# Optimization experiments

Hardware: AMD Instinct MI355X
Metric: run time of the kernel (lower is better)

## Reference

```python
import jax, jax.numpy as jnp
import numpy as np

C_M = 256
C = 32
C_Z = 128
EPS = 1e-5


def setup_inputs() -> dict:
    key = jax.random.key(0)
    ks = jax.random.split(key, 8)
    b, s, i = 1, 128, 256
    msa = jax.random.normal(ks[0], (b, s, i, C_M), dtype=jnp.float32)
    scale_in = 1.0 / np.sqrt(C_M)
    scale_out = 1.0 / np.sqrt(C * C)
    return {
        "msa_representation": msa,
        "ln_w": jnp.ones((C_M,), jnp.float32),
        "ln_b": jnp.zeros((C_M,), jnp.float32),
        "w_left": jax.random.normal(ks[1], (C_M, C), jnp.float32) * scale_in,
        "b_left": jax.random.normal(ks[2], (C,), jnp.float32) * scale_in,
        "w_right": jax.random.normal(ks[3], (C_M, C), jnp.float32) * scale_in,
        "b_right": jax.random.normal(ks[4], (C,), jnp.float32) * scale_in,
        "w_out": jax.random.normal(ks[5], (C * C, C_Z), jnp.float32) * scale_out,
        "b_out": jax.random.normal(ks[6], (C_Z,), jnp.float32) * scale_out,
    }


def reference(msa_representation, ln_w, ln_b, w_left, b_left, w_right, b_right, w_out, b_out):
    x = msa_representation
    # LayerNorm over c_m
    mu = jnp.mean(x, axis=-1, keepdims=True)
    var = jnp.mean(jnp.square(x - mu), axis=-1, keepdims=True)
    x = (x - mu) * jax.lax.rsqrt(var + EPS) * ln_w + ln_b
    # dual projections: [b, s, i, c]
    A = x @ w_left + b_left
    B = x @ w_right + b_right
    s_dim = x.shape[1]
    # outer product mean over MSA depth s: [b, i, j, c, c]
    outer = jnp.einsum('bsic,bsjd->bijcd', A, B) / s_dim
    b_, i_, j_ = outer.shape[0], outer.shape[1], outer.shape[2]
    flat = outer.reshape(b_, i_, j_, C * C)
    return flat @ w_out + b_out
```

## Files before the change

### kernel.cpp

```cpp
#include <hip/hip_runtime.h>

typedef __attribute__((ext_vector_type(8))) short short8;
typedef __attribute__((ext_vector_type(4))) float f32x4;

#define CM 256
#define CC 32
#define CZ 128
#define SDIM 128
#define IDIM 256

__device__ __forceinline__ unsigned short f2bf(float f) {
  union { float f; unsigned u; } v; v.f = f;
  unsigned r = v.u + 0x7fffu + ((v.u >> 16) & 1u);
  return (unsigned short)(r >> 16);
}
__device__ __forceinline__ unsigned pack_bf2(float a, float b) {
  union { float f; unsigned u; } x, y; x.f = a; y.f = b;
  return ((x.u + 0x8000u) >> 16) | ((y.u + 0x8000u) & 0xffff0000u);
}

__global__ void k_prep(const float* __restrict__ wl, const float* __restrict__ wr,
                       const float* __restrict__ wo,
                       unsigned short* __restrict__ wlrT2, unsigned short* __restrict__ WF) {
  int t = blockIdx.x * 256 + threadIdx.x;
  if (t < 2048) {
    int frag = t >> 6, lane = t & 63;
    int nt = frag >> 3, ks = frag & 7;
    int ln = lane & 15, qd = lane >> 4;
    int c64 = nt * 16 + ln;
#pragma unroll
    for (int e = 0; e < 8; ++e) {
      int cm = ks * 32 + qd * 8 + e;
      float v = (c64 < CC) ? wl[cm * CC + c64] : wr[cm * CC + (c64 - CC)];
      wlrT2[(size_t)t * 8 + e] = f2bf(v);
    }
  } else {
    int t2 = t - 2048;
    if (t2 < 8 * 32 * 64) {
      int zt = t2 >> 11, ks = (t2 >> 6) & 31, lane = t2 & 63;
      int ln = lane & 15, qd = lane >> 4;
      int z = zt * 16 + ln;
#pragma unroll
      for (int e = 0; e < 8; ++e) {
        int c = qd * 8 + e, d = ks;
        WF[(size_t)t2 * 8 + e] = f2bf(wo[(c * 32 + d) * CZ + z] * (1.0f / 128.0f));
      }
    }
  }
}

__global__ __launch_bounds__(512) void k_lnproj(
    const float* __restrict__ x, const float* __restrict__ lnw, const float* __restrict__ lnb,
    const float* __restrict__ bl, const float* __restrict__ br,
    const unsigned short* __restrict__ wlrT2,
    unsigned short* __restrict__ A2, unsigned short* __restrict__ Bbuf) {
  __shared__ __align__(16) unsigned short xn[64][264];
  __shared__ __align__(16) unsigned short sT[64][72];
  int tid = threadIdx.x;
  int lane = tid & 63, ww = tid >> 6;
  int qd = lane >> 4, ln = lane & 15;
  int i = blockIdx.x, sh = blockIdx.y;

  float4 w4 = ((const float4*)lnw)[lane];
  float4 b4 = ((const float4*)lnb)[lane];

#pragma unroll
  for (int rr = 0; rr < 8; ++rr) {
    int sl = ww * 8 + rr;
    int s = sh * 64 + sl;
    float4 v = ((const float4*)(x + ((size_t)s * IDIM + i) * CM))[lane];
    float s1 = v.x + v.y + v.z + v.w;
    float s2 = v.x * v.x + v.y * v.y + v.z * v.z + v.w * v.w;
#pragma unroll
    for (int off = 32; off; off >>= 1) {
      s1 += __shfl_xor(s1, off);
      s2 += __shfl_xor(s2, off);
    }
    float mu = s1 * (1.0f / 256.0f);
    float var = s2 * (1.0f / 256.0f) - mu * mu;
    float rs = rsqrtf(var + 1e-5f);
    ushort4 h;
    h.x = f2bf((v.x - mu) * rs * w4.x + b4.x);
    h.y = f2bf((v.y - mu) * rs * w4.y + b4.y);
    h.z = f2bf((v.z - mu) * rs * w4.z + b4.z);
    h.w = f2bf((v.w - mu) * rs * w4.w + b4.w);
    *(ushort4*)&xn[sl][lane * 4] = h;
  }
  __syncthreads();

  int mt = ww >> 1, nh = ww & 1;
  f32x4 acc[2];
#pragma unroll
  for (int t = 0; t < 2; ++t) acc[t] = (f32x4){0.f, 0.f, 0.f, 0.f};
#pragma unroll
  for (int ks = 0; ks < 8; ++ks) {
    short8 af = *(const short8*)&xn[mt * 16 + ln][ks * 32 + qd * 8];
#pragma unroll
    for (int t = 0; t < 2; ++t) {
      int nt = nh * 2 + t;
      short8 bf = *(const short8*)(wlrT2 + ((size_t)((nt * 8 + ks) * 64 + lane)) * 8);
      acc[t] = __builtin_amdgcn_mfma_f32_16x16x32_bf16(af, bf, acc[t], 0, 0, 0);
    }
  }
#pragma unroll
  for (int t = 0; t < 2; ++t) {
    int nt = nh * 2 + t;
    int c64 = nt * 16 + ln;
    float bias = (c64 < CC) ? bl[c64] : br[c64 - CC];
    ushort4 h;
    h.x = f2bf(acc[t][0] + bias);
    h.y = f2bf(acc[t][1] + bias);
    h.z = f2bf(acc[t][2] + bias);
    h.w = f2bf(acc[t][3] + bias);
    *(ushort4*)&sT[c64][mt * 16 + qd * 4] = h;
  }
  __syncthreads();

  if (ww < 4) {
    int rtloc = ww >> 1, ksl = ww & 1;
    short8 v = *(const short8*)&sT[rtloc * 16 + ln][ksl * 32 + qd * 8];
    *(short8*)(A2 + ((size_t)(((2 * i + rtloc) * 4 + (sh * 2 + ksl)) * 64 + lane)) * 8) = v;
  } else {
    int t2 = tid - 256;
    int row = t2 >> 3, ch = t2 & 7;
    short8 v = *(const short8*)&sT[CC + row][ch * 8];
    *(short8*)(Bbuf + ((size_t)(i * CC + row)) * SDIM + sh * 64 + ch * 8) = v;
  }
}

__global__ __launch_bounds__(512, 2) void k_main(
    const unsigned short* __restrict__ A2, const unsigned short* __restrict__ Bbuf,
    const unsigned short* __restrict__ WF, const float* __restrict__ bout,
    float* __restrict__ out) {
  extern __shared__ __align__(16) char lds[];
  unsigned short* sPA = (unsigned short*)lds;
  unsigned short* sPB = (unsigned short*)(lds + 66048);
  unsigned short* sB  = (unsigned short*)(lds + 132096);
  float* redR = (float*)lds;
  int tid = threadIdx.x;
  int lane = tid & 63, ww = tid >> 6;
  int qd = lane >> 4, ln = lane & 15;
  int bx = blockIdx.x;
  int itile = (bx & 7) * 4 + ((bx >> 3) & 3);
  int jg = bx >> 5;
  int i0 = itile * 8;
  int ztp = ww & 3, kq = ww >> 2;

  short8 afp[2][4];
#pragma unroll
  for (int ti = 0; ti < 2; ++ti)
#pragma unroll
    for (int ks = 0; ks < 4; ++ks)
      afp[ti][ks] =
          *(const short8*)(A2 + ((size_t)((i0 * 2 + ww * 2 + ti) * 4 + ks) * 64 + lane) * 8);

  short8 bpre[2];
#pragma unroll
  for (int tt = 0; tt < 2; ++tt) {
    int idx = tid + tt * 512;
    int r = idx >> 4, ch = idx & 15;
    bpre[tt] = *(const short8*)(Bbuf + ((size_t)(jg * 256 + r)) * SDIM + ch * 8);
  }

#pragma unroll
  for (int q = 0; q < 4; ++q) {
#pragma unroll
    for (int tt = 0; tt < 2; ++tt) {
      int idx = tid + tt * 512;
      int r = idx >> 4, ch = idx & 15;
      *(short8*)&sB[r * 136 + ch * 8] = bpre[tt];
    }
    __syncthreads();
    if (q < 3) {
#pragma unroll
      for (int tt = 0; tt < 2; ++tt) {
        int idx = tid + tt * 512;
        int r = idx >> 4, ch = idx & 15;
        bpre[tt] = *(const short8*)(Bbuf + ((size_t)(jg * 256 + (q + 1) * 64 + r)) * SDIM + ch * 8);
      }
    }
    unsigned short* sP = (q & 2) ? sPB : sPA;
    f32x4 acc1[2][4];
#pragma unroll
    for (int a = 0; a < 2; ++a)
#pragma unroll
      for (int b = 0; b < 4; ++b) acc1[a][b] = (f32x4){0.f, 0.f, 0.f, 0.f};
#pragma unroll
    for (int ks = 0; ks < 4; ++ks)
#pragma unroll
      for (int tjj = 0; tjj < 4; ++tjj) {
        short8 bf = *(const short8*)&sB[(tjj * 16 + ln) * 136 + ks * 32 + qd * 8];
#pragma unroll
        for (int ti = 0; ti < 2; ++ti)
          acc1[ti][tjj] =
              __builtin_amdgcn_mfma_f32_16x16x32_bf16(afp[ti][ks], bf, acc1[ti][tjj], 0, 0, 0);
      }
    __syncthreads();
#pragma unroll
    for (int ti = 0; ti < 2; ++ti) {
      int cbase = 16 * ti + qd * 4;
      int cb = cbase >> 3;
#pragma unroll
      for (int tjj = 0; tjj < 4; ++tjj) {
        int d = 16 * (tjj & 1) + ln;
        int p = ww * 4 + 2 * (q & 1) + (tjj >> 1);
        uint2 u;
        u.x = pack_bf2(acc1[ti][tjj][0], acc1[ti][tjj][1]);
        u.y = pack_bf2(acc1[ti][tjj][2], acc1[ti][tjj][3]);
        *(uint2*)&sP[p * 1032 + d * 32 + ((((d >> 1) & 3) ^ cb) * 8) + (cbase & 7)] = u;
      }
    }
  }
  __syncthreads();

  f32x4 acc2[2][2][2];
#pragma unroll
  for (int a = 0; a < 2; ++a)
#pragma unroll
    for (int b = 0; b < 2; ++b)
#pragma unroll
      for (int c = 0; c < 2; ++c) acc2[a][b][c] = (f32x4){0.f, 0.f, 0.f, 0.f};
#pragma unroll
  for (int cc = 0; cc < 16; ++cc) {
    int ks = kq * 16 + cc;
    int swz = ((((ks >> 1) & 3) ^ qd) * 8);
    short8 afr[2][2];
#pragma unroll
    for (int mt = 0; mt < 2; ++mt) {
      afr[0][mt] = *(const short8*)&sPA[(mt * 16 + ln) * 1032 + ks * 32 + swz];
      afr[1][mt] = *(const short8*)&sPB[(mt * 16 + ln) * 1032 + ks * 32 + swz];
    }
#pragma unroll
    for (int h2 = 0; h2 < 2; ++h2) {
      int zt = ztp * 2 + h2;
      short8 bfr = *(const short8*)(WF + ((size_t)(zt * 32 + ks) * 64 + lane) * 8);
#pragma unroll
      for (int tb = 0; tb < 2; ++tb)
#pragma unroll
        for (int mt = 0; mt < 2; ++mt)
          acc2[tb][h2][mt] = __builtin_amdgcn_mfma_f32_16x16x32_bf16(bfr, afr[tb][mt],
                                                                    acc2[tb][h2][mt], 0, 0, 0);
    }
  }
  __syncthreads();

  if (kq == 1) {
#pragma unroll
    for (int tb = 0; tb < 2; ++tb)
#pragma unroll
      for (int h2 = 0; h2 < 2; ++h2)
#pragma unroll
        for (int mt = 0; mt < 2; ++mt)
          *(f32x4*)&redR[((((tb * 4 + ztp) * 2 + h2) * 2 + mt) << 8) + lane * 4] =
              acc2[tb][h2][mt];
  }
  __syncthreads();
  if (kq == 0) {
#pragma unroll
    for (int tb = 0; tb < 2; ++tb)
#pragma unroll
      for (int h2 = 0; h2 < 2; ++h2) {
        int z = (ztp * 2 + h2) * 16 + qd * 4;
        f32x4 bz = *(const f32x4*)(bout + z);
#pragma unroll
        for (int mt = 0; mt < 2; ++mt) {
          int p = mt * 16 + ln;
          f32x4 v = acc2[tb][h2][mt] +
                    *(const f32x4*)&redR[((((tb * 4 + ztp) * 2 + h2) * 2 + mt) << 8) + lane * 4] +
                    bz;
          int i = i0 + (p >> 2), j = jg * 8 + tb * 4 + (p & 3);
          *(f32x4*)&out[((size_t)i * IDIM + j) * CZ + z] = v;
        }
      }
  }
}

extern "C" void kernel_launch(void* const* d_in, const int* in_sizes, int n_in,
                              void* d_out, int out_size, void* d_ws, size_t ws_size,
                              hipStream_t stream) {
  const float* msa = (const float*)d_in[0];
  const float* lnw = (const float*)d_in[1];
  const float* lnb = (const float*)d_in[2];
  const float* wl  = (const float*)d_in[3];
  const float* bl  = (const float*)d_in[4];
  const float* wr  = (const float*)d_in[5];
  const float* br  = (const float*)d_in[6];
  const float* wo  = (const float*)d_in[7];
  const float* bo  = (const float*)d_in[8];
  float* out = (float*)d_out;

  char* ws = (char*)d_ws;
  unsigned short* A2    = (unsigned short*)ws;
  unsigned short* Bbuf  = (unsigned short*)(ws + (2u << 20));
  unsigned short* wlrT2 = (unsigned short*)(ws + (4u << 20));
  unsigned short* WF    = (unsigned short*)(ws + (4u << 20) + 32768);

  (void)hipFuncSetAttribute((const void*)k_main,
                            hipFuncAttributeMaxDynamicSharedMemorySize, 149504);

  k_prep<<<72, 256, 0, stream>>>(wl, wr, wo, wlrT2, WF);
  k_lnproj<<<dim3(256, 2), 512, 0, stream>>>(msa, lnw, lnb, bl, br, wlrT2, A2, Bbuf);
  k_main<<<1024, 512, 149504, stream>>>(A2, Bbuf, WF, bo, out);
}
```

Measured before the change: 144.5 us.

## Halve j-tile per block to cut LDS and double grid, add MFMA priority

Each k_main block now covers 4 j columns instead of 8, so the two P buffers in shared memory become one and the B staging holds 32 rows instead of 64. Dynamic LDS drops from about 146 KB to about 73 KB and the grid doubles to 2048 blocks, so more blocks can be resident per CU. MFMA loops are wrapped in s_setprio to favour matrix issue. The trade-off is that each block's A fragments and W_out fragments are now reused across half as many j columns, which doubles global and L2 traffic for those operands.

```diff
diff --git a/kernel.cpp b/kernel.cpp
--- a/kernel.cpp
+++ b/kernel.cpp
@@ -133,9 +133,8 @@
     const unsigned short* __restrict__ WF, const float* __restrict__ bout,
     float* __restrict__ out) {
   extern __shared__ __align__(16) char lds[];
-  unsigned short* sPA = (unsigned short*)lds;
-  unsigned short* sPB = (unsigned short*)(lds + 66048);
-  unsigned short* sB  = (unsigned short*)(lds + 132096);
+  unsigned short* sP = (unsigned short*)lds;
+  unsigned short* sB = (unsigned short*)(lds + 66048);
   float* redR = (float*)lds;
   int tid = threadIdx.x;
   int lane = tid & 63, ww = tid >> 6;
@@ -154,56 +153,49 @@
       afp[ti][ks] =
           *(const short8*)(A2 + ((size_t)((i0 * 2 + ww * 2 + ti) * 4 + ks) * 64 + lane) * 8);
 
-  short8 bpre[2];
-#pragma unroll
-  for (int tt = 0; tt < 2; ++tt) {
-    int idx = tid + tt * 512;
-    int r = idx >> 4, ch = idx & 15;
-    bpre[tt] = *(const short8*)(Bbuf + ((size_t)(jg * 256 + r)) * SDIM + ch * 8);
+  short8 bpre;
+  {
+    int r = tid >> 4, ch = tid & 15;
+    bpre = *(const short8*)(Bbuf + ((size_t)(jg * 4) * CC + r) * SDIM + ch * 8);
   }
 
 #pragma unroll
   for (int q = 0; q < 4; ++q) {
-#pragma unroll
-    for (int tt = 0; tt < 2; ++tt) {
-      int idx = tid + tt * 512;
-      int r = idx >> 4, ch = idx & 15;
-      *(short8*)&sB[r * 136 + ch * 8] = bpre[tt];
+    {
+      int r = tid >> 4, ch = tid & 15;
+      *(short8*)&sB[r * 136 + ch * 8] = bpre;
     }
     __syncthreads();
     if (q < 3) {
-#pragma unroll
-      for (int tt = 0; tt < 2; ++tt) {
-        int idx = tid + tt * 512;
-        int r = idx >> 4, ch = idx & 15;
-        bpre[tt] = *(const short8*)(Bbuf + ((size_t)(jg * 256 + (q + 1) * 64 + r)) * SDIM + ch * 8);
-      }
-    }
-    unsigned short* sP = (q & 2) ? sPB : sPA;
-    f32x4 acc1[2][4];
+      int r = tid >> 4, ch = tid & 15;
+      bpre = *(const short8*)(Bbuf + ((size_t)(jg * 4 + q + 1) * CC + r) * SDIM + ch * 8);
+    }
+    f32x4 acc1[2][2];
 #pragma unroll
     for (int a = 0; a < 2; ++a)
 #pragma unroll
-      for (int b = 0; b < 4; ++b) acc1[a][b] = (f32x4){0.f, 0.f, 0.f, 0.f};
+      for (int b = 0; b < 2; ++b) acc1[a][b] = (f32x4){0.f, 0.f, 0.f, 0.f};
+    __builtin_amdgcn_s_setprio(1);
 #pragma unroll
     for (int ks = 0; ks < 4; ++ks)
 #pragma unroll
-      for (int tjj = 0; tjj < 4; ++tjj) {
+      for (int tjj = 0; tjj < 2; ++tjj) {
         short8 bf = *(const short8*)&sB[(tjj * 16 + ln) * 136 + ks * 32 + qd * 8];
 #pragma unroll
         for (int ti = 0; ti < 2; ++ti)
           acc1[ti][tjj] =
               __builtin_amdgcn_mfma_f32_16x16x32_bf16(afp[ti][ks], bf, acc1[ti][tjj], 0, 0, 0);
       }
+    __builtin_amdgcn_s_setprio(0);
     __syncthreads();
 #pragma unroll
     for (int ti = 0; ti < 2; ++ti) {
       int cbase = 16 * ti + qd * 4;
       int cb = cbase >> 3;
 #pragma unroll
-      for (int tjj = 0; tjj < 4; ++tjj) {
-        int d = 16 * (tjj & 1) + ln;
-        int p = ww * 4 + 2 * (q & 1) + (tjj >> 1);
+      for (int tjj = 0; tjj < 2; ++tjj) {
+        int d = 16 * tjj + ln;
+        int p = ww * 4 + q;
         uint2 u;
         u.x = pack_bf2(acc1[ti][tjj][0], acc1[ti][tjj][1]);
         u.y = pack_bf2(acc1[ti][tjj][2], acc1[ti][tjj][3]);
@@ -213,65 +205,55 @@
   }
   __syncthreads();
 
-  f32x4 acc2[2][2][2];
+  f32x4 acc2[2][2];
 #pragma unroll
   for (int a = 0; a < 2; ++a)
 #pragma unroll
-    for (int b = 0; b < 2; ++b)
-#pragma unroll
-      for (int c = 0; c < 2; ++c) acc2[a][b][c] = (f32x4){0.f, 0.f, 0.f, 0.f};
+    for (int b = 0; b < 2; ++b) acc2[a][b] = (f32x4){0.f, 0.f, 0.f, 0.f};
+  __builtin_amdgcn_s_setprio(1);
 #pragma unroll
   for (int cc = 0; cc < 16; ++cc) {
     int ks = kq * 16 + cc;
     int swz = ((((ks >> 1) & 3) ^ qd) * 8);
-    short8 afr[2][2];
-#pragma unroll
-    for (int mt = 0; mt < 2; ++mt) {
-      afr[0][mt] = *(const short8*)&sPA[(mt * 16 + ln) * 1032 + ks * 32 + swz];
-      afr[1][mt] = *(const short8*)&sPB[(mt * 16 + ln) * 1032 + ks * 32 + swz];
-    }
+    short8 afr[2];
+#pragma unroll
+    for (int mt = 0; mt < 2; ++mt)
+      afr[mt] = *(const short8*)&sP[(mt * 16 + ln) * 1032 + ks * 32 + swz];
 #pragma unroll
     for (int h2 = 0; h2 < 2; ++h2) {
       int zt = ztp * 2 + h2;
       short8 bfr = *(const short8*)(WF + ((size_t)(zt * 32 + ks) * 64 + lane) * 8);
 #pragma unroll
-      for (int tb = 0; tb < 2; ++tb)
-#pragma unroll
-        for (int mt = 0; mt < 2; ++mt)
-          acc2[tb][h2][mt] = __builtin_amdgcn_mfma_f32_16x16x32_bf16(bfr, afr[tb][mt],
-                                                                    acc2[tb][h2][mt], 0, 0, 0);
-    }
-  }
+      for (int mt = 0; mt < 2; ++mt)
+        acc2[h2][mt] =
+            __builtin_amdgcn_mfma_f32_16x16x32_bf16(bfr, afr[mt], acc2[h2][mt], 0, 0, 0);
+    }
+  }
+  __builtin_amdgcn_s_setprio(0);
   __syncthreads();
 
   if (kq == 1) {
 #pragma unroll
-    for (int tb = 0; tb < 2; ++tb)
-#pragma unroll
-      for (int h2 = 0; h2 < 2; ++h2)
-#pragma unroll
-        for (int mt = 0; mt < 2; ++mt)
-          *(f32x4*)&redR[((((tb * 4 + ztp) * 2 + h2) * 2 + mt) << 8) + lane * 4] =
-              acc2[tb][h2][mt];
+    for (int h2 = 0; h2 < 2; ++h2)
+#pragma unroll
+      for (int mt = 0; mt < 2; ++mt)
+        *(f32x4*)&redR[(((ztp * 2 + h2) * 2 + mt) << 8) + lane * 4] = acc2[h2][mt];
   }
   __syncthreads();
   if (kq == 0) {
 #pragma unroll
-    for (int tb = 0; tb < 2; ++tb)
-#pragma unroll
-      for (int h2 = 0; h2 < 2; ++h2) {
-        int z = (ztp * 2 + h2) * 16 + qd * 4;
-        f32x4 bz = *(const f32x4*)(bout + z);
-#pragma unroll
-        for (int mt = 0; mt < 2; ++mt) {
-          int p = mt * 16 + ln;
-          f32x4 v = acc2[tb][h2][mt] +
-                    *(const f32x4*)&redR[((((tb * 4 + ztp) * 2 + h2) * 2 + mt) << 8) + lane * 4] +
-                    bz;
-          int i = i0 + (p >> 2), j = jg * 8 + tb * 4 + (p & 3);
-          *(f32x4*)&out[((size_t)i * IDIM + j) * CZ + z] = v;
-        }
-      }
+    for (int h2 = 0; h2 < 2; ++h2) {
+      int z = (ztp * 2 + h2) * 16 + qd * 4;
+      f32x4 bz = *(const f32x4*)(bout + z);
+#pragma unroll
+      for (int mt = 0; mt < 2; ++mt) {
+        int p = mt * 16 + ln;
+        f32x4 v = acc2[h2][mt] +
+                  *(const f32x4*)&redR[(((ztp * 2 + h2) * 2 + mt) << 8) + lane * 4] + bz;
+        int i = i0 + (p >> 2), j = jg * 4 + (p & 3);
+        *(f32x4*)&out[((size_t)i * IDIM + j) * CZ + z] = v;
+      }
+    }
   }
 }
 
@@ -296,9 +278,9 @@
   unsigned short* WF    = (unsigned short*)(ws + (4u << 20) + 32768);
 
   (void)hipFuncSetAttribute((const void*)k_main,
-                            hipFuncAttributeMaxDynamicSharedMemorySize, 149504);
+                            hipFuncAttributeMaxDynamicSharedMemorySize, 74752);
 
   k_prep<<<72, 256, 0, stream>>>(wl, wr, wo, wlrT2, WF);
   k_lnproj<<<dim3(256, 2), 512, 0, stream>>>(msa, lnw, lnb, bl, br, wlrT2, A2, Bbuf);
-  k_main<<<1024, 512, 149504, stream>>>(A2, Bbuf, WF, bo, out);
-}
+  k_main<<<2048, 512, 74752, stream>>>(A2, Bbuf, WF, bo, out);
+}
```

Result: no change. 143.0 us (-1.1%).
